# Kernel tuning notes

Measured on AMD Instinct MI355X. Metric: run time of the kernel, lower is better.

## Reference

```python
import jax, jax.numpy as jnp
import numpy as np

N_NEIGHBOR = 8


def setup_inputs() -> dict:
    key = jax.random.key(0)
    k1, k2, k3 = jax.random.split(key, 3)
    B, n_shape, D = 2048, 64, 64
    S = n_shape * N_NEIGHBOR  # 512 neighbor slots
    drug = jax.random.normal(k1, (B, n_shape, D), dtype=jnp.float32)
    rel = jax.random.normal(k2, (B, S, D), dtype=jnp.float32)
    ent = jax.random.normal(k3, (B, S, D), dtype=jnp.float32)
    return {"drug": drug, "rel": rel, "ent": ent}


def reference(drug, rel, ent):
    # drug: [B, n_shape, D]; rel, ent: [B, n_shape*n_neighbor, D]
    B, S, D = rel.shape
    n_shape = S // N_NEIGHBOR
    rel4 = rel.reshape(B, n_shape, N_NEIGHBOR, D)
    ent4 = ent.reshape(B, n_shape, N_NEIGHBOR, D)
    # relation score: dot(drug, rel) per neighbor, broadcast drug over neighbor axis
    score = jnp.einsum('bgd,bgnd->bgn', drug, rel4)  # [B, n_shape, n_neighbor]
    # weighted sum of neighbor entity embeddings over the neighbor axis
    out = jnp.einsum('bgn,bgnd->bgd', score, ent4)  # [B, n_shape, D]
    return out
```

## Files before the change

kernel.cpp:

```cpp
#include <hip/hip_runtime.h>


constexpr int BATCH   = 2048;
constexpr int NSHAPE  = 64;
constexpr int DIM     = 64;
constexpr int NGROUPS = BATCH * NSHAPE;
constexpr int WAVES_PER_BLOCK = 4;

__global__ __launch_bounds__(256) void kgnn_head_kernel(
    const float* __restrict__ drug,
    const float* __restrict__ rel,
    const float* __restrict__ ent,
    float*       __restrict__ out)
{
    const int gid  = (int)((blockIdx.x * blockDim.x + threadIdx.x) >> 6);
    const int lane = threadIdx.x & 63;

    const float4* drug4 = reinterpret_cast<const float4*>(drug + (size_t)gid * DIM);
    const float4* rel4  = reinterpret_cast<const float4*>(rel  + (size_t)gid * (8 * DIM));
    const float4* ent4  = reinterpret_cast<const float4*>(ent  + (size_t)gid * (8 * DIM));

    const int seg = lane >> 4;
    const int pos = lane & 15;
    (void)seg;

    const float4 dg = drug4[pos];

    float4 acc = make_float4(0.f, 0.f, 0.f, 0.f);

    #pragma unroll
    for (int pass = 0; pass < 2; ++pass) {
        const float4 r = rel4[pass * 64 + lane];
        const float4 e = ent4[pass * 64 + lane];

        float p = dg.x * r.x + dg.y * r.y + dg.z * r.z + dg.w * r.w;

        p += __shfl_xor(p, 1);
        p += __shfl_xor(p, 2);
        p += __shfl_xor(p, 4);
        p += __shfl_xor(p, 8);

        acc.x = fmaf(p, e.x, acc.x);
        acc.y = fmaf(p, e.y, acc.y);
        acc.z = fmaf(p, e.z, acc.z);
        acc.w = fmaf(p, e.w, acc.w);
    }

    acc.x += __shfl_xor(acc.x, 16);
    acc.y += __shfl_xor(acc.y, 16);
    acc.z += __shfl_xor(acc.z, 16);
    acc.w += __shfl_xor(acc.w, 16);
    acc.x += __shfl_xor(acc.x, 32);
    acc.y += __shfl_xor(acc.y, 32);
    acc.z += __shfl_xor(acc.z, 32);
    acc.w += __shfl_xor(acc.w, 32);

    if (lane < 16) {
        float4* o4 = reinterpret_cast<float4*>(out + (size_t)gid * DIM);
        o4[pos] = acc;
    }
}

extern "C" void kernel_launch(void* const* d_in, const int* in_sizes, int n_in,
                              void* d_out, int out_size, void* d_ws, size_t ws_size,
                              hipStream_t stream) {
    const float* drug = (const float*)d_in[0];
    const float* rel  = (const float*)d_in[1];
    const float* ent  = (const float*)d_in[2];
    float* out = (float*)d_out;

    const int blocks = NGROUPS / WAVES_PER_BLOCK;
    kgnn_head_kernel<<<blocks, WAVES_PER_BLOCK * 64, 0, stream>>>(drug, rel, ent, out);
}
```

Baseline: 110.3 us.

## Process eight groups per wave with register double-buffered prefetch

Each wave now handles eight consecutive groups instead of one. It prefetches the next group's drug, rel and ent vectors into registers while computing the current one. The grid shrinks by a factor of eight, which amortizes launch and wave setup and keeps more loads in flight per wave. The risk is lower occupancy and fewer waves to hide latency in a purely bandwidth-bound kernel.

```diff
diff --git a/kernel.cpp b/kernel.cpp
--- a/kernel.cpp
+++ b/kernel.cpp
@@ -5,6 +5,7 @@
 constexpr int NSHAPE  = 64;
 constexpr int DIM     = 64;
 constexpr int NGROUPS = BATCH * NSHAPE;
+constexpr int GPW     = 8;
 constexpr int WAVES_PER_BLOCK = 4;
 
 __global__ __launch_bounds__(256) void kgnn_head_kernel(
@@ -13,51 +14,62 @@
     const float* __restrict__ ent,
     float*       __restrict__ out)
 {
-    const int gid  = (int)((blockIdx.x * blockDim.x + threadIdx.x) >> 6);
-    const int lane = threadIdx.x & 63;
+    const int wave_id = (int)((blockIdx.x * blockDim.x + threadIdx.x) >> 6);
+    const int lane    = threadIdx.x & 63;
+    const int pos     = lane & 15;
 
-    const float4* drug4 = reinterpret_cast<const float4*>(drug + (size_t)gid * DIM);
-    const float4* rel4  = reinterpret_cast<const float4*>(rel  + (size_t)gid * (8 * DIM));
-    const float4* ent4  = reinterpret_cast<const float4*>(ent  + (size_t)gid * (8 * DIM));
+    const int g0 = wave_id * GPW;
 
-    const int seg = lane >> 4;
-    const int pos = lane & 15;
-    (void)seg;
+    const float4* drug4 = reinterpret_cast<const float4*>(drug);
+    const float4* rel4  = reinterpret_cast<const float4*>(rel);
+    const float4* ent4  = reinterpret_cast<const float4*>(ent);
+    float4*       out4  = reinterpret_cast<float4*>(out);
 
-    const float4 dg = drug4[pos];
-
-    float4 acc = make_float4(0.f, 0.f, 0.f, 0.f);
+    float4 dg = drug4[(size_t)g0 * 16 + pos];
+    float4 r0 = rel4[(size_t)g0 * 128 + lane];
+    float4 r1 = rel4[(size_t)g0 * 128 + 64 + lane];
+    float4 e0 = ent4[(size_t)g0 * 128 + lane];
+    float4 e1 = ent4[(size_t)g0 * 128 + 64 + lane];
 
     #pragma unroll
-    for (int pass = 0; pass < 2; ++pass) {
-        const float4 r = rel4[pass * 64 + lane];
-        const float4 e = ent4[pass * 64 + lane];
+    for (int k = 0; k < GPW; ++k) {
+        const float4 dgc = dg, r0c = r0, r1c = r1, e0c = e0, e1c = e1;
 
-        float p = dg.x * r.x + dg.y * r.y + dg.z * r.z + dg.w * r.w;
+        if (k + 1 < GPW) {
+            const size_t g = (size_t)(g0 + k + 1);
+            dg = drug4[g * 16 + pos];
+            r0 = rel4[g * 128 + lane];
+            r1 = rel4[g * 128 + 64 + lane];
+            e0 = ent4[g * 128 + lane];
+            e1 = ent4[g * 128 + 64 + lane];
+        }
 
-        p += __shfl_xor(p, 1);
-        p += __shfl_xor(p, 2);
-        p += __shfl_xor(p, 4);
-        p += __shfl_xor(p, 8);
+        float p0 = dgc.x * r0c.x + dgc.y * r0c.y + dgc.z * r0c.z + dgc.w * r0c.w;
+        float p1 = dgc.x * r1c.x + dgc.y * r1c.y + dgc.z * r1c.z + dgc.w * r1c.w;
 
-        acc.x = fmaf(p, e.x, acc.x);
-        acc.y = fmaf(p, e.y, acc.y);
-        acc.z = fmaf(p, e.z, acc.z);
-        acc.w = fmaf(p, e.w, acc.w);
-    }
+        p0 += __shfl_xor(p0, 1);  p1 += __shfl_xor(p1, 1);
+        p0 += __shfl_xor(p0, 2);  p1 += __shfl_xor(p1, 2);
+        p0 += __shfl_xor(p0, 4);  p1 += __shfl_xor(p1, 4);
+        p0 += __shfl_xor(p0, 8);  p1 += __shfl_xor(p1, 8);
 
-    acc.x += __shfl_xor(acc.x, 16);
-    acc.y += __shfl_xor(acc.y, 16);
-    acc.z += __shfl_xor(acc.z, 16);
-    acc.w += __shfl_xor(acc.w, 16);
-    acc.x += __shfl_xor(acc.x, 32);
-    acc.y += __shfl_xor(acc.y, 32);
-    acc.z += __shfl_xor(acc.z, 32);
-    acc.w += __shfl_xor(acc.w, 32);
+        float4 acc;
+        acc.x = fmaf(p0, e0c.x, p1 * e1c.x);
+        acc.y = fmaf(p0, e0c.y, p1 * e1c.y);
+        acc.z = fmaf(p0, e0c.z, p1 * e1c.z);
+        acc.w = fmaf(p0, e0c.w, p1 * e1c.w);
 
-    if (lane < 16) {
-        float4* o4 = reinterpret_cast<float4*>(out + (size_t)gid * DIM);
-        o4[pos] = acc;
+        acc.x += __shfl_xor(acc.x, 16);
+        acc.y += __shfl_xor(acc.y, 16);
+        acc.z += __shfl_xor(acc.z, 16);
+        acc.w += __shfl_xor(acc.w, 16);
+        acc.x += __shfl_xor(acc.x, 32);
+        acc.y += __shfl_xor(acc.y, 32);
+        acc.z += __shfl_xor(acc.z, 32);
+        acc.w += __shfl_xor(acc.w, 32);
+
+        if (lane < 16) {
+            out4[(size_t)(g0 + k) * 16 + pos] = acc;
+        }
     }
 }
 
@@ -69,6 +81,6 @@
     const float* ent  = (const float*)d_in[2];
     float* out = (float*)d_out;
 
-    const int blocks = NGROUPS / WAVES_PER_BLOCK;
+    const int blocks = NGROUPS / (GPW * WAVES_PER_BLOCK);
     kgnn_head_kernel<<<blocks, WAVES_PER_BLOCK * 64, 0, stream>>>(drug, rel, ent, out);
 }
```

Result: slower. 118.4 us (+7.3%).
